# Performance work log

Measured on AMD Instinct MI355X. Metric: run time of the kernel, lower is better.

## Reference

```python
import jax, jax.numpy as jnp
import numpy as np

N_NODES = 50000
N_EDGES = 1600000
IN_DIM = 128
HIDDEN = 256
N_CLASSES = 2
N_GRAPHS = 512
BN_EPS = 1e-5


def setup_inputs() -> dict:
    key = jax.random.key(0)
    ks = jax.random.split(key, 12)
    x = jax.random.normal(ks[0], (N_NODES, IN_DIM), dtype=jnp.float32)
    edge_index = jax.random.randint(ks[1], (2, N_EDGES), 0, N_NODES, dtype=jnp.int64)
    batch = jnp.sort(jax.random.randint(ks[2], (N_NODES,), 0, N_GRAPHS, dtype=jnp.int64))
    s1 = 1.0 / np.sqrt(IN_DIM)
    s2 = 1.0 / np.sqrt(HIDDEN)
    return {
        "x": x,
        "edge_index": edge_index,
        "batch": batch,
        # GIN MLP: Linear(in,hidden) -> BN -> ReLU -> Linear(hidden,hidden)
        "W1": jax.random.uniform(ks[3], (IN_DIM, HIDDEN), jnp.float32, -s1, s1),
        "b1": jnp.zeros((HIDDEN,), jnp.float32),
        "g1": jnp.ones((HIDDEN,), jnp.float32),
        "be1": jnp.zeros((HIDDEN,), jnp.float32),
        "W2": jax.random.uniform(ks[4], (HIDDEN, HIDDEN), jnp.float32, -s2, s2),
        "b2": jnp.zeros((HIDDEN,), jnp.float32),
        # attention gate: Linear(hidden, 1)
        "Wg": jax.random.uniform(ks[5], (HIDDEN, 1), jnp.float32, -s2, s2),
        "bg": jnp.zeros((1,), jnp.float32),
        # head: BN(hidden) -> Dropout(eval: identity) -> Linear(hidden, n_classes)
        "g2": jnp.ones((HIDDEN,), jnp.float32),
        "be2": jnp.zeros((HIDDEN,), jnp.float32),
        "Wh": jax.random.uniform(ks[6], (HIDDEN, N_CLASSES), jnp.float32, -s2, s2),
        "bh": jnp.zeros((N_CLASSES,), jnp.float32),
    }


def _batchnorm(h, gamma, beta):
    # training-mode BN: batch statistics over axis 0 (biased variance, as torch)
    mu = jnp.mean(h, axis=0)
    var = jnp.mean(jnp.square(h - mu), axis=0)
    return gamma * (h - mu) * jax.lax.rsqrt(var + BN_EPS) + beta


def reference(x, edge_index, batch, W1, b1, g1, be1, W2, b2, Wg, bg, g2, be2, Wh, bh):
    src, dst = edge_index[0], edge_index[1]
    # GINConv (eps=0): agg_i = sum_{j->i} x_j ; h = MLP(x + agg)
    agg = jax.ops.segment_sum(x[src], dst, num_segments=N_NODES)  # [N, in_dim]
    h = x + agg
    h = h @ W1 + b1                      # [N, hidden]
    h = jax.nn.relu(_batchnorm(h, g1, be1))
    h = h @ W2 + b2                      # [N, hidden]
    h = jax.nn.relu(h)                   # outer F.relu in forward
    # AttentionalAggregation: segment softmax of gate, weighted sum per graph
    gate = h @ Wg + bg                   # [N, 1]
    m = jax.ops.segment_max(gate, batch, num_segments=N_GRAPHS)  # [G, 1]
    e = jnp.exp(gate - m[batch])
    s = jax.ops.segment_sum(e, batch, num_segments=N_GRAPHS)     # [G, 1]
    alpha = e / s[batch]                 # [N, 1]
    pooled = jax.ops.segment_sum(alpha * h, batch, num_segments=N_GRAPHS)  # [G, hidden]
    # head: BN -> (Dropout eval = identity) -> Linear -> log_softmax
    z = _batchnorm(pooled, g2, be2) @ Wh + bh  # [G, n_classes]
    return jax.nn.log_softmax(z, axis=-1)
```

## Files before the change

kernel.cpp:

```cpp
#include <hip/hip_runtime.h>

typedef unsigned int u32;
typedef unsigned short ushort_t;
typedef __attribute__((ext_vector_type(8))) short bf16x8;
typedef __attribute__((ext_vector_type(4))) float f32x4;

__device__ __forceinline__ float bf2f_lo(u32 u){
  union{u32 i; float f;} v; v.i = u<<16; return v.f;
}
__device__ __forceinline__ float bf2f_hi(u32 u){
  union{u32 i; float f;} v; v.i = u & 0xFFFF0000u; return v.f;
}
__device__ __forceinline__ float bf2f_s(ushort_t u){
  union{u32 i; float f;} v; v.i = ((u32)u)<<16; return v.f;
}
__device__ __forceinline__ u32 pack2bf(float a, float b){
  union{float f; u32 i;} va, vb; va.f=a; vb.f=b;
  u32 ra = (va.i + 0x7FFF + ((va.i>>16)&1)) >> 16;
  u32 rb = (vb.i + 0x7FFF + ((vb.i>>16)&1)) & 0xFFFF0000u;
  return ra | rb;
}
__device__ __forceinline__ ushort_t f2bf1(float f){
  union{float f; u32 i;} v; v.f=f;
  u32 r = v.i + 0x7FFF + ((v.i>>16)&1);
  return (ushort_t)(r>>16);
}

__global__ __launch_bounds__(256) void to_bf16(const float* __restrict__ x, u32* __restrict__ xb, long n4){
  long i = (long)blockIdx.x*256 + threadIdx.x;
  if(i*4 >= n4*4) return;
  float4 v = ((const float4*)x)[i];
  uint2 o; o.x = pack2bf(v.x, v.y); o.y = pack2bf(v.z, v.w);
  ((uint2*)xb)[i] = o;
}

__global__ __launch_bounds__(256) void transpose_w(const float* __restrict__ W, ushort_t* __restrict__ Wt, int K){
  int n = blockIdx.x;
  for(int k = threadIdx.x; k < K; k += 256){
    Wt[(size_t)n*K + k] = f2bf1(W[(size_t)k*256 + n]);
  }
}

__global__ __launch_bounds__(256) void hist_k(const int* __restrict__ dst, int* __restrict__ bcount,
                                              int E, int N, int NB){
  __shared__ int h[1024];
  for(int i=threadIdx.x; i<1024; i+=256) h[i]=0;
  __syncthreads();
  int e0 = blockIdx.x*8192;
  int e1 = min(e0+8192, E);
  for(int i=e0+threadIdx.x; i<e1; i+=256){
    int d = dst[i];
    if((u32)d >= (u32)N) d = 0;
    atomicAdd(&h[d>>6], 1);
  }
  __syncthreads();
  for(int i=threadIdx.x; i<NB; i+=256){
    int v = h[i];
    if(v) atomicAdd(&bcount[i], v);
  }
}

__global__ __launch_bounds__(256) void bucket_scan(const int* __restrict__ bcount, int* __restrict__ bstart,
                                                   int* __restrict__ bcursor, int* __restrict__ offs,
                                                   int NB, int N, int E){
  __shared__ int tsum[256];
  int t = threadIdx.x;
  int base = t*4;
  int a0 = (base+0<NB)?bcount[base+0]:0;
  int a1 = (base+1<NB)?bcount[base+1]:0;
  int a2 = (base+2<NB)?bcount[base+2]:0;
  int a3 = (base+3<NB)?bcount[base+3]:0;
  int s0=a0, s1=s0+a1, s2=s1+a2, s3=s2+a3;
  tsum[t]=s3; __syncthreads();
  #pragma unroll
  for(int d=1; d<256; d<<=1){
    int v = (t>=d)?tsum[t-d]:0;
    __syncthreads();
    tsum[t]+=v;
    __syncthreads();
  }
  int prev = (t>0)?tsum[t-1]:0;
  if(base+0<NB){ bstart[base+0]=prev;    bcursor[(base+0)*16]=0; }
  if(base+1<NB){ bstart[base+1]=prev+s0; bcursor[(base+1)*16]=0; }
  if(base+2<NB){ bstart[base+2]=prev+s1; bcursor[(base+2)*16]=0; }
  if(base+3<NB){ bstart[base+3]=prev+s2; bcursor[(base+3)*16]=0; }
  if(t==255){ bstart[NB]=prev+s3; offs[N]=E; }
}

__global__ __launch_bounds__(256) void binscatter2(const int* __restrict__ src, const int* __restrict__ dst,
                                                   const int* __restrict__ bstart, int* __restrict__ bcursor,
                                                   u32* __restrict__ pairs, int E, int N, int NB){
  __shared__ int hist[1024];
  __shared__ int base[1024];
  int e0 = blockIdx.x*8192;
  int e1 = min(e0+8192, E);
  for(int i=threadIdx.x; i<NB; i+=256) hist[i]=0;
  __syncthreads();
  for(int i=e0+threadIdx.x; i<e1; i+=256){
    int d = dst[i];
    if((u32)d >= (u32)N) d = 0;
    atomicAdd(&hist[d>>6], 1);
  }
  __syncthreads();
  for(int i=threadIdx.x; i<NB; i+=256){
    int c = hist[i];
    base[i] = c ? (bstart[i] + atomicAdd(&bcursor[i*16], c)) : 0;
    hist[i] = 0;
  }
  __syncthreads();
  for(int i=e0+threadIdx.x; i<e1; i+=256){
    int d = dst[i]; if((u32)d >= (u32)N) d = 0;
    int s = src[i]; if((u32)s >= (u32)N) s = 0;
    int b = d>>6;
    int loc = atomicAdd(&hist[b], 1);
    pairs[base[b]+loc] = (u32)s | (((u32)(d & 63))<<17);
  }
}

__global__ __launch_bounds__(256) void bucket_csr(const u32* __restrict__ pairs, const int* __restrict__ bstart,
                                                  int* __restrict__ offs, int* __restrict__ elist, int N){
  __shared__ int dcnt[64];
  __shared__ int dcur[64];
  int b = blockIdx.x;
  int p0 = bstart[b], p1 = bstart[b+1];
  if(threadIdx.x < 64) dcnt[threadIdx.x] = 0;
  __syncthreads();
  for(int i=p0+threadIdx.x; i<p1; i+=256){
    u32 u = pairs[i];
    atomicAdd(&dcnt[u>>17], 1);
  }
  __syncthreads();
  if(threadIdx.x == 0){
    int running = p0;
    #pragma unroll
    for(int j=0;j<64;j++){
      dcur[j] = running;
      int node = b*64 + j;
      if(node < N) offs[node] = running;
      running += dcnt[j];
    }
  }
  __syncthreads();
  for(int i=p0+threadIdx.x; i<p1; i+=256){
    u32 u = pairs[i];
    int pos = atomicAdd(&dcur[u>>17], 1);
    elist[pos] = (int)(u & 0x1FFFFu);
  }
}

__global__ __launch_bounds__(256) void gather_sum_bf(const u32* __restrict__ xb, const int* __restrict__ offs,
                                                     const int* __restrict__ elist, u32* __restrict__ h0b,
                                                     int N, int E){
  int slot = threadIdx.x >> 4;
  int c = threadIdx.x & 15;
  int i = blockIdx.x*16 + slot;
  if(i >= N) return;
  const uint4* xr = (const uint4*)xb;
  uint4 xv = xr[(size_t)i*16 + c];
  float acc[8] = {
    bf2f_lo(xv.x), bf2f_hi(xv.x), bf2f_lo(xv.y), bf2f_hi(xv.y),
    bf2f_lo(xv.z), bf2f_hi(xv.z), bf2f_lo(xv.w), bf2f_hi(xv.w) };
  int e0 = offs[i], e1 = offs[i+1];
  e0 = max(0, min(e0, E));
  e1 = max(e0, min(e1, E));
  int j = e0;
  for(; j+4 <= e1; j += 4){
    int s0 = elist[j+0]; if((u32)s0 >= (u32)N) s0 = 0;
    int s1 = elist[j+1]; if((u32)s1 >= (u32)N) s1 = 0;
    int s2 = elist[j+2]; if((u32)s2 >= (u32)N) s2 = 0;
    int s3 = elist[j+3]; if((u32)s3 >= (u32)N) s3 = 0;
    uint4 v0 = xr[(size_t)s0*16 + c];
    uint4 v1 = xr[(size_t)s1*16 + c];
    uint4 v2 = xr[(size_t)s2*16 + c];
    uint4 v3 = xr[(size_t)s3*16 + c];
    acc[0]+=bf2f_lo(v0.x); acc[1]+=bf2f_hi(v0.x); acc[2]+=bf2f_lo(v0.y); acc[3]+=bf2f_hi(v0.y);
    acc[4]+=bf2f_lo(v0.z); acc[5]+=bf2f_hi(v0.z); acc[6]+=bf2f_lo(v0.w); acc[7]+=bf2f_hi(v0.w);
    acc[0]+=bf2f_lo(v1.x); acc[1]+=bf2f_hi(v1.x); acc[2]+=bf2f_lo(v1.y); acc[3]+=bf2f_hi(v1.y);
    acc[4]+=bf2f_lo(v1.z); acc[5]+=bf2f_hi(v1.z); acc[6]+=bf2f_lo(v1.w); acc[7]+=bf2f_hi(v1.w);
    acc[0]+=bf2f_lo(v2.x); acc[1]+=bf2f_hi(v2.x); acc[2]+=bf2f_lo(v2.y); acc[3]+=bf2f_hi(v2.y);
    acc[4]+=bf2f_lo(v2.z); acc[5]+=bf2f_hi(v2.z); acc[6]+=bf2f_lo(v2.w); acc[7]+=bf2f_hi(v2.w);
    acc[0]+=bf2f_lo(v3.x); acc[1]+=bf2f_hi(v3.x); acc[2]+=bf2f_lo(v3.y); acc[3]+=bf2f_hi(v3.y);
    acc[4]+=bf2f_lo(v3.z); acc[5]+=bf2f_hi(v3.z); acc[6]+=bf2f_lo(v3.w); acc[7]+=bf2f_hi(v3.w);
  }
  for(; j < e1; j++){
    int s = elist[j];
    if((u32)s >= (u32)N) s = 0;
    uint4 v = xr[(size_t)s*16 + c];
    acc[0]+=bf2f_lo(v.x); acc[1]+=bf2f_hi(v.x);
    acc[2]+=bf2f_lo(v.y); acc[3]+=bf2f_hi(v.y);
    acc[4]+=bf2f_lo(v.z); acc[5]+=bf2f_hi(v.z);
    acc[6]+=bf2f_lo(v.w); acc[7]+=bf2f_hi(v.w);
  }
  uint4 o;
  o.x = pack2bf(acc[0],acc[1]); o.y = pack2bf(acc[2],acc[3]);
  o.z = pack2bf(acc[4],acc[5]); o.w = pack2bf(acc[6],acc[7]);
  ((uint4*)h0b)[(size_t)i*16 + c] = o;
}

template<int K, bool BNA, bool RELUOUT, bool GATE, bool ABF16, bool OUTBF16>
__global__ __launch_bounds__(512) void gemm_mfma(const void* __restrict__ Ap, const ushort_t* __restrict__ Wt,
                                                 const float* __restrict__ bias,
                                                 const float* __restrict__ scale, const float* __restrict__ shift,
                                                 void* __restrict__ Cp, int M,
                                                 const float* __restrict__ Wg, const float* __restrict__ bg,
                                                 float* __restrict__ gate){
  __shared__ uint4 Al[8*129];
  __shared__ uint4 Bl[8*257];
  __shared__ float gacc[128];
  const int tid  = threadIdx.x;
  const int lane = tid & 63;
  const int wave = tid >> 6;
  const int lm   = lane & 15;
  const int q    = lane >> 4;
  const int mhalf= wave >> 2;
  const int nq   = wave & 3;
  const int m0   = blockIdx.x * 128;

  if(GATE && tid < 128) gacc[tid] = 0.f;

  f32x4 acc[4][4];
  #pragma unroll
  for(int i=0;i<4;i++)
    #pragma unroll
    for(int j=0;j<4;j++) acc[i][j] = (f32x4){0.f,0.f,0.f,0.f};

  for(int k0=0; k0<K; k0+=64){
    #pragma unroll
    for(int i=0;i<2;i++){
      int idx = tid*2 + i;
      int m = idx >> 3, c = idx & 7;
      int grow = m0 + m;
      int kk = k0 + c*8;
      uint4 v = make_uint4(0,0,0,0);
      if(ABF16){
        if(grow < M) v = *(const uint4*)((const ushort_t*)Ap + (size_t)grow*K + kk);
        if(BNA){
          float f0=bf2f_lo(v.x), f1=bf2f_hi(v.x), f2=bf2f_lo(v.y), f3=bf2f_hi(v.y);
          float f4=bf2f_lo(v.z), f5=bf2f_hi(v.z), f6=bf2f_lo(v.w), f7=bf2f_hi(v.w);
          float4 s0 = *(const float4*)(scale+kk),  s1 = *(const float4*)(scale+kk+4);
          float4 t0 = *(const float4*)(shift+kk),  t1 = *(const float4*)(shift+kk+4);
          f0=fmaxf(fmaf(s0.x,f0,t0.x),0.f); f1=fmaxf(fmaf(s0.y,f1,t0.y),0.f);
          f2=fmaxf(fmaf(s0.z,f2,t0.z),0.f); f3=fmaxf(fmaf(s0.w,f3,t0.w),0.f);
          f4=fmaxf(fmaf(s1.x,f4,t1.x),0.f); f5=fmaxf(fmaf(s1.y,f5,t1.y),0.f);
          f6=fmaxf(fmaf(s1.z,f6,t1.z),0.f); f7=fmaxf(fmaf(s1.w,f7,t1.w),0.f);
          v.x = pack2bf(f0,f1); v.y = pack2bf(f2,f3);
          v.z = pack2bf(f4,f5); v.w = pack2bf(f6,f7);
        }
      } else {
        float4 u0 = make_float4(0,0,0,0), u1 = make_float4(0,0,0,0);
        if(grow < M){
          u0 = *(const float4*)((const float*)Ap + (size_t)grow*K + kk);
          u1 = *(const float4*)((const float*)Ap + (size_t)grow*K + kk + 4);
        }
        if(BNA){
          float4 s0 = *(const float4*)(scale+kk),  s1 = *(const float4*)(scale+kk+4);
          float4 t0 = *(const float4*)(shift+kk),  t1 = *(const float4*)(shift+kk+4);
          u0.x=fmaxf(fmaf(s0.x,u0.x,t0.x),0.f); u0.y=fmaxf(fmaf(s0.y,u0.y,t0.y),0.f);
          u0.z=fmaxf(fmaf(s0.z,u0.z,t0.z),0.f); u0.w=fmaxf(fmaf(s0.w,u0.w,t0.w),0.f);
          u1.x=fmaxf(fmaf(s1.x,u1.x,t1.x),0.f); u1.y=fmaxf(fmaf(s1.y,u1.y,t1.y),0.f);
          u1.z=fmaxf(fmaf(s1.z,u1.z,t1.z),0.f); u1.w=fmaxf(fmaf(s1.w,u1.w,t1.w),0.f);
        }
        v.x = pack2bf(u0.x,u0.y); v.y = pack2bf(u0.z,u0.w);
        v.z = pack2bf(u1.x,u1.y); v.w = pack2bf(u1.z,u1.w);
      }
      Al[c*129 + m] = v;
    }
    #pragma unroll
    for(int i=0;i<4;i++){
      int idx = tid*4 + i;
      int n = idx >> 3, c = idx & 7;
      Bl[c*257 + n] = *(const uint4*)(Wt + (size_t)n*K + k0 + c*8);
    }
    __syncthreads();
    #pragma unroll
    for(int ks=0; ks<2; ks++){
      int cc = ks*4 + q;
      bf16x8 af[4], bfr[4];
      #pragma unroll
      for(int mi=0; mi<4; mi++)
        af[mi] = *((const bf16x8*)&Al[cc*129 + mhalf*64 + mi*16 + lm]);
      #pragma unroll
      for(int ni=0; ni<4; ni++)
        bfr[ni] = *((const bf16x8*)&Bl[cc*257 + nq*64 + ni*16 + lm]);
      #pragma unroll
      for(int mi=0; mi<4; mi++)
        #pragma unroll
        for(int ni=0; ni<4; ni++)
          acc[mi][ni] = __builtin_amdgcn_mfma_f32_16x16x32_bf16(af[mi], bfr[ni], acc[mi][ni], 0, 0, 0);
    }
    __syncthreads();
  }

  float bb[4], wgv[4];
  #pragma unroll
  for(int ni=0; ni<4; ni++){
    int col = nq*64 + ni*16 + lm;
    bb[ni] = bias[col];
    if(GATE) wgv[ni] = Wg[col];
  }
  #pragma unroll
  for(int mi=0; mi<4; mi++){
    int rowloc0 = mhalf*64 + mi*16 + q*4;
    float gp[4] = {0.f,0.f,0.f,0.f};
    #pragma unroll
    for(int ni=0; ni<4; ni++){
      int col = nq*64 + ni*16 + lm;
      f32x4 o = acc[mi][ni];
      #pragma unroll
      for(int r=0; r<4; r++){
        float v = o[r] + bb[ni];
        if(RELUOUT) v = fmaxf(v, 0.f);
        int row = m0 + rowloc0 + r;
        if(row < M){
          if(OUTBF16) ((ushort_t*)Cp)[(size_t)row*256 + col] = f2bf1(v);
          else        ((float*)Cp)[(size_t)row*256 + col] = v;
        }
        if(GATE) gp[r] = fmaf(v, wgv[ni], gp[r]);
      }
    }
    if(GATE){
      #pragma unroll
      for(int r=0; r<4; r++){
        if(m0 + rowloc0 + r < M) atomicAdd(&gacc[rowloc0 + r], gp[r]);
      }
    }
  }
  if(GATE){
    __syncthreads();
    if(tid < 128){
      int row = m0 + tid;
      if(row < M) gate[row] = gacc[tid] + bg[0];
    }
  }
}

__global__ __launch_bounds__(256) void col_stats_bf(const u32* __restrict__ h, float* __restrict__ psum,
                                                    float* __restrict__ pq, int M, int rpb, int nblk){
  int b = blockIdx.x;
  int g = threadIdx.x >> 6;
  int lane = threadIdx.x & 63;
  int c0 = lane*4;
  int r0 = b*rpb;
  int r1 = min(r0+rpb, M);
  float4 s4 = make_float4(0.f,0.f,0.f,0.f);
  float4 q4 = make_float4(0.f,0.f,0.f,0.f);
  for(int r=r0+g; r<r1; r+=4){
    uint2 u = *(const uint2*)(h + (size_t)r*128 + lane*2);
    float v0=bf2f_lo(u.x), v1=bf2f_hi(u.x), v2=bf2f_lo(u.y), v3=bf2f_hi(u.y);
    s4.x+=v0; s4.y+=v1; s4.z+=v2; s4.w+=v3;
    q4.x=fmaf(v0,v0,q4.x); q4.y=fmaf(v1,v1,q4.y);
    q4.z=fmaf(v2,v2,q4.z); q4.w=fmaf(v3,v3,q4.w);
  }
  __shared__ float ls[1024];
  __shared__ float lq[1024];
  *(float4*)&ls[g*256+c0] = s4;
  *(float4*)&lq[g*256+c0] = q4;
  __syncthreads();
  if(threadIdx.x < 64){
    #pragma unroll
    for(int j=0;j<4;j++){
      int c = c0+j;
      float s = ls[c]+ls[256+c]+ls[512+c]+ls[768+c];
      float q = lq[c]+lq[256+c]+lq[512+c]+lq[768+c];
      psum[(size_t)c*nblk + b] = s;
      pq[(size_t)c*nblk + b]   = q;
    }
  }
}

__global__ __launch_bounds__(256) void col_stats2(const float* __restrict__ h, float* __restrict__ psum,
                                                  float* __restrict__ pq, int M, int rpb, int nblk){
  int b = blockIdx.x;
  int g = threadIdx.x >> 6;
  int lane = threadIdx.x & 63;
  int c0 = lane*4;
  int r0 = b*rpb;
  int r1 = min(r0+rpb, M);
  float4 s4 = make_float4(0.f,0.f,0.f,0.f);
  float4 q4 = make_float4(0.f,0.f,0.f,0.f);
  for(int r=r0+g; r<r1; r+=4){
    float4 v = *(const float4*)(h + (size_t)r*256 + c0);
    s4.x+=v.x; s4.y+=v.y; s4.z+=v.z; s4.w+=v.w;
    q4.x=fmaf(v.x,v.x,q4.x); q4.y=fmaf(v.y,v.y,q4.y);
    q4.z=fmaf(v.z,v.z,q4.z); q4.w=fmaf(v.w,v.w,q4.w);
  }
  __shared__ float ls[1024];
  __shared__ float lq[1024];
  *(float4*)&ls[g*256+c0] = s4;
  *(float4*)&lq[g*256+c0] = q4;
  __syncthreads();
  if(threadIdx.x < 64){
    #pragma unroll
    for(int j=0;j<4;j++){
      int c = c0+j;
      float s = ls[c]+ls[256+c]+ls[512+c]+ls[768+c];
      float q = lq[c]+lq[256+c]+lq[512+c]+lq[768+c];
      psum[(size_t)c*nblk + b] = s;
      pq[(size_t)c*nblk + b]   = q;
    }
  }
}

__global__ __launch_bounds__(512) void stats_fin(const float* __restrict__ psum, const float* __restrict__ pq,
                                                 const float* __restrict__ gamma, const float* __restrict__ beta,
                                                 float* __restrict__ scale, float* __restrict__ shift,
                                                 int nblk, float invM){
  __shared__ float red[512];
  int t = threadIdx.x;
  const float* src = (t<256) ? (psum + (size_t)t*nblk) : (pq + (size_t)(t-256)*nblk);
  float s = 0.f;
  for(int i=0;i<nblk;i+=4){
    float4 v = *(const float4*)(src+i);
    s += v.x+v.y+v.z+v.w;
  }
  red[t]=s; __syncthreads();
  if(t<256){
    float mu  = red[t]*invM;
    float var = fmaxf(red[256+t]*invM - mu*mu, 0.f);
    float sc  = gamma[t] * rsqrtf(var + 1e-5f);
    scale[t]=sc; shift[t]=fmaf(-mu, sc, beta[t]);
  }
}

__global__ __launch_bounds__(256) void pool_k(const ushort_t* __restrict__ h2b, const float* __restrict__ gate,
                                              const int* __restrict__ batch, float* __restrict__ pooled, int N){
  int g = blockIdx.x;
  __shared__ int sb[2];
  __shared__ float red[4];
  __shared__ float s_m, s_inv;
  if(threadIdx.x < 2){
    int target = g + threadIdx.x;
    int lo=0, hi=N;
    while(lo<hi){ int mid=(lo+hi)>>1; if(batch[mid] < target) lo=mid+1; else hi=mid; }
    sb[threadIdx.x] = lo;
  }
  __syncthreads();
  int beg = sb[0], end = sb[1];
  float mx = -1e30f;
  for(int i=beg+threadIdx.x; i<end; i+=256) mx = fmaxf(mx, gate[i]);
  #pragma unroll
  for(int d=32; d>0; d>>=1) mx = fmaxf(mx, __shfl_down(mx, d, 64));
  if((threadIdx.x&63)==0) red[threadIdx.x>>6] = mx;
  __syncthreads();
  if(threadIdx.x==0) s_m = fmaxf(fmaxf(red[0],red[1]), fmaxf(red[2],red[3]));
  __syncthreads();
  float m = s_m;
  float s = 0.f;
  for(int i=beg+threadIdx.x; i<end; i+=256) s += expf(gate[i]-m);
  #pragma unroll
  for(int d=32; d>0; d>>=1) s += __shfl_down(s, d, 64);
  if((threadIdx.x&63)==0) red[threadIdx.x>>6] = s;
  __syncthreads();
  if(threadIdx.x==0){
    float tot = red[0]+red[1]+red[2]+red[3];
    s_inv = (tot > 0.f) ? 1.f/tot : 0.f;
  }
  __syncthreads();
  float inv = s_inv;
  int t = threadIdx.x;
  float acc = 0.f;
  int i = beg;
  for(; i+2 <= end; i += 2){
    float a0 = expf(gate[i]-m) * inv;
    float a1 = expf(gate[i+1]-m) * inv;
    float h0 = bf2f_s(h2b[(size_t)i*256 + t]);
    float h1 = bf2f_s(h2b[(size_t)(i+1)*256 + t]);
    acc = fmaf(a0, h0, acc);
    acc = fmaf(a1, h1, acc);
  }
  for(; i < end; i++){
    float a = expf(gate[i]-m) * inv;
    acc = fmaf(a, bf2f_s(h2b[(size_t)i*256 + t]), acc);
  }
  pooled[g*256 + t] = acc;
}

__global__ __launch_bounds__(256) void head_k(const float* __restrict__ pooled,
                                              const float* __restrict__ sc2, const float* __restrict__ sh2,
                                              const float* __restrict__ Wh, const float* __restrict__ bh,
                                              float* __restrict__ out, int G){
  int w = (blockIdx.x*256 + threadIdx.x) >> 6;
  int l = threadIdx.x & 63;
  if(w >= G) return;
  float4 v  = *(const float4*)(pooled + (size_t)w*256 + l*4);
  float4 sc = *(const float4*)(sc2 + l*4);
  float4 sh = *(const float4*)(sh2 + l*4);
  float vv[4] = { fmaf(sc.x,v.x,sh.x), fmaf(sc.y,v.y,sh.y), fmaf(sc.z,v.z,sh.z), fmaf(sc.w,v.w,sh.w) };
  float4 w0 = *(const float4*)(Wh + (size_t)l*8);
  float4 w1 = *(const float4*)(Wh + (size_t)l*8 + 4);
  float a0 = vv[0]*w0.x + vv[1]*w0.z + vv[2]*w1.x + vv[3]*w1.z;
  float a1 = vv[0]*w0.y + vv[1]*w0.w + vv[2]*w1.y + vv[3]*w1.w;
  #pragma unroll
  for(int d=32; d>0; d>>=1){ a0 += __shfl_down(a0,d,64); a1 += __shfl_down(a1,d,64); }
  if(l==0){
    float z0 = a0 + bh[0];
    float z1 = a1 + bh[1];
    float mz = fmaxf(z0,z1);
    float lse = mz + logf(expf(z0-mz) + expf(z1-mz));
    out[w*2]   = z0 - lse;
    out[w*2+1] = z1 - lse;
  }
}

extern "C" void kernel_launch(void* const* d_in, const int* in_sizes, int n_in,
                              void* d_out, int out_size, void* d_ws, size_t ws_size,
                              hipStream_t stream){
  const float* x   = (const float*)d_in[0];
  const int*   ei  = (const int*)d_in[1];
  const int*   bat = (const int*)d_in[2];
  const float* W1  = (const float*)d_in[3];
  const float* b1  = (const float*)d_in[4];
  const float* g1  = (const float*)d_in[5];
  const float* be1 = (const float*)d_in[6];
  const float* W2  = (const float*)d_in[7];
  const float* b2  = (const float*)d_in[8];
  const float* Wg  = (const float*)d_in[9];
  const float* bg  = (const float*)d_in[10];
  const float* g2  = (const float*)d_in[11];
  const float* be2 = (const float*)d_in[12];
  const float* Wh  = (const float*)d_in[13];
  const float* bh  = (const float*)d_in[14];

  const int N = in_sizes[0] / 128;
  const int E = in_sizes[1] / 2;
  const int G = out_size / 2;
  const int NB = (N + 63) >> 6;
  const int NBLK1 = 512;
  const int NBLK2 = 64;

  char* ws = (char*)d_ws;
  u32*   h0b    = (u32*)ws;
  u32*   xb     = (u32*)(ws + 12800000);
  int*   elist  = (int*)(ws + 25600000);
  u32*   pairs  = (u32*)(ws + 32000000);
  int*   offs   = (int*)(ws + 38400000);
  int*   bcount = (int*)(ws + 38600192);
  int*   bstart = (int*)(ws + 38604288);
  int*   bcursor= (int*)(ws + 38608640);
  ushort_t* h2b = (ushort_t*)ws;
  u32*   h1b    = (u32*)(ws + 51200000);
  char*  p2 = ws + 102400000;
  float* psum1 = (float*)p2;          p2 += 256*NBLK1*4;
  float* pq1   = (float*)p2;          p2 += 256*NBLK1*4;
  float* psum2 = (float*)p2;          p2 += 256*NBLK2*4;
  float* pq2   = (float*)p2;          p2 += 256*NBLK2*4;
  float* sc1   = (float*)p2;          p2 += 1024;
  float* sh1   = (float*)p2;          p2 += 1024;
  float* gate  = (float*)p2;          p2 += (size_t)N*4 + 256;
  float* pooled= (float*)p2;          p2 += (size_t)G*256*4;
  float* sc2   = (float*)p2;          p2 += 1024;
  float* sh2   = (float*)p2;          p2 += 1024;
  ushort_t* W1t = (ushort_t*)p2;      p2 += 256*128*2;
  ushort_t* W2t = (ushort_t*)p2;      p2 += 256*256*2;

  const int* src = ei;
  const int* dst = ei + E;

  hipMemsetAsync(bcount, 0, (size_t)NB*4, stream);

  transpose_w<<<256, 256, 0, stream>>>(W1, W1t, 128);
  transpose_w<<<256, 256, 0, stream>>>(W2, W2t, 256);
  long n4 = (long)N*128/4;
  to_bf16    <<<(int)((n4+255)/256), 256, 0, stream>>>(x, xb, n4);

  int nchunk = (E + 8191)/8192;
  hist_k     <<<nchunk, 256, 0, stream>>>(dst, bcount, E, N, NB);
  bucket_scan<<<1, 256, 0, stream>>>(bcount, bstart, bcursor, offs, NB, N, E);
  binscatter2<<<nchunk, 256, 0, stream>>>(src, dst, bstart, bcursor, pairs, E, N, NB);
  bucket_csr <<<NB, 256, 0, stream>>>(pairs, bstart, offs, elist, N);
  gather_sum_bf<<<(N+15)/16, 256, 0, stream>>>(xb, offs, elist, h0b, N, E);

  int gblocks = (N + 127)/128;
  gemm_mfma<128,false,false,false,true,true><<<gblocks, 512, 0, stream>>>(
      h0b, W1t, b1, nullptr, nullptr, h1b, N, nullptr, nullptr, nullptr);
  int rpb1 = (N + NBLK1 - 1)/NBLK1;
  col_stats_bf <<<NBLK1, 256, 0, stream>>>(h1b, psum1, pq1, N, rpb1, NBLK1);
  stats_fin  <<<1, 512, 0, stream>>>(psum1, pq1, g1, be1, sc1, sh1, NBLK1, 1.0f/(float)N);
  gemm_mfma<256,true,true,true,true,true><<<gblocks, 512, 0, stream>>>(
      h1b, W2t, b2, sc1, sh1, h2b, N, Wg, bg, gate);

  pool_k <<<G, 256, 0, stream>>>(h2b, gate, bat, pooled, N);
  int rpb2 = (G + NBLK2 - 1)/NBLK2;
  col_stats2 <<<NBLK2, 256, 0, stream>>>(pooled, psum2, pq2, G, rpb2, NBLK2);
  stats_fin  <<<1, 512, 0, stream>>>(psum2, pq2, g2, be2, sc2, sh2, NBLK2, 1.0f/(float)G);
  head_k <<<(G+3)/4, 256, 0, stream>>>(pooled, sc2, sh2, Wh, bh, (float*)d_out, G);
}
```

Measured before the change: 362.9 us.

## Fuse bucket CSR build into gather and rework attention pooling

Merges the per-bucket CSR construction and the neighbor gather into one kernel. Each block sorts its bucket's edges into shared memory and then gathers the source rows directly, which removes the global elist/offs writes and reads and one kernel launch. The gather unrolls by 8 for more memory-level parallelism, and falls back to a slow linear scan when a bucket holds more than 4096 edges. Separately, pool_k moves to 512 threads, precomputes attention weights per chunk in shared memory and splits the rows across two halves, so the exp is computed once per node instead of once per thread.

```diff
diff --git a/kernel.cpp b/kernel.cpp
--- a/kernel.cpp
+++ b/kernel.cpp
@@ -61,8 +61,7 @@
 }
 
 __global__ __launch_bounds__(256) void bucket_scan(const int* __restrict__ bcount, int* __restrict__ bstart,
-                                                   int* __restrict__ bcursor, int* __restrict__ offs,
-                                                   int NB, int N, int E){
+                                                   int* __restrict__ bcursor, int NB){
   __shared__ int tsum[256];
   int t = threadIdx.x;
   int base = t*4;
@@ -84,7 +83,7 @@
   if(base+1<NB){ bstart[base+1]=prev+s0; bcursor[(base+1)*16]=0; }
   if(base+2<NB){ bstart[base+2]=prev+s1; bcursor[(base+2)*16]=0; }
   if(base+3<NB){ bstart[base+3]=prev+s2; bcursor[(base+3)*16]=0; }
-  if(t==255){ bstart[NB]=prev+s3; offs[N]=E; }
+  if(t==255){ bstart[NB]=prev+s3; }
 }
 
 __global__ __launch_bounds__(256) void binscatter2(const int* __restrict__ src, const int* __restrict__ dst,
@@ -117,84 +116,110 @@
   }
 }
 
-__global__ __launch_bounds__(256) void bucket_csr(const u32* __restrict__ pairs, const int* __restrict__ bstart,
-                                                  int* __restrict__ offs, int* __restrict__ elist, int N){
+#define BCAP 4096
+__global__ __launch_bounds__(256) void gather_bucket(const u32* __restrict__ xb,
+                                                     const u32* __restrict__ pairs,
+                                                     const int* __restrict__ bstart,
+                                                     u32* __restrict__ h0b, int N){
+  __shared__ int lsrc[BCAP];
   __shared__ int dcnt[64];
+  __shared__ int dstart[65];
   __shared__ int dcur[64];
   int b = blockIdx.x;
   int p0 = bstart[b], p1 = bstart[b+1];
-  if(threadIdx.x < 64) dcnt[threadIdx.x] = 0;
-  __syncthreads();
-  for(int i=p0+threadIdx.x; i<p1; i+=256){
-    u32 u = pairs[i];
-    atomicAdd(&dcnt[u>>17], 1);
-  }
-  __syncthreads();
-  if(threadIdx.x == 0){
-    int running = p0;
-    #pragma unroll
-    for(int j=0;j<64;j++){
-      dcur[j] = running;
-      int node = b*64 + j;
-      if(node < N) offs[node] = running;
-      running += dcnt[j];
-    }
-  }
-  __syncthreads();
-  for(int i=p0+threadIdx.x; i<p1; i+=256){
-    u32 u = pairs[i];
-    int pos = atomicAdd(&dcur[u>>17], 1);
-    elist[pos] = (int)(u & 0x1FFFFu);
-  }
-}
-
-__global__ __launch_bounds__(256) void gather_sum_bf(const u32* __restrict__ xb, const int* __restrict__ offs,
-                                                     const int* __restrict__ elist, u32* __restrict__ h0b,
-                                                     int N, int E){
-  int slot = threadIdx.x >> 4;
-  int c = threadIdx.x & 15;
-  int i = blockIdx.x*16 + slot;
-  if(i >= N) return;
+  int cnt = p1 - p0;
+  int tid = threadIdx.x;
+  if(tid < 64) dcnt[tid] = 0;
+  __syncthreads();
+  bool fits = (cnt <= BCAP) && (cnt >= 0);
+  if(fits){
+    for(int i=tid; i<cnt; i+=256){
+      u32 u = pairs[p0+i];
+      atomicAdd(&dcnt[(u>>17)&63], 1);
+    }
+    __syncthreads();
+    if(tid==0){
+      int run=0;
+      #pragma unroll
+      for(int j=0;j<64;j++){ dstart[j]=run; dcur[j]=run; run+=dcnt[j]; }
+      dstart[64]=run;
+    }
+    __syncthreads();
+    for(int i=tid; i<cnt; i+=256){
+      u32 u = pairs[p0+i];
+      int pos = atomicAdd(&dcur[(u>>17)&63], 1);
+      lsrc[pos] = (int)(u & 0x1FFFFu);
+    }
+    __syncthreads();
+  }
   const uint4* xr = (const uint4*)xb;
-  uint4 xv = xr[(size_t)i*16 + c];
-  float acc[8] = {
-    bf2f_lo(xv.x), bf2f_hi(xv.x), bf2f_lo(xv.y), bf2f_hi(xv.y),
-    bf2f_lo(xv.z), bf2f_hi(xv.z), bf2f_lo(xv.w), bf2f_hi(xv.w) };
-  int e0 = offs[i], e1 = offs[i+1];
-  e0 = max(0, min(e0, E));
-  e1 = max(e0, min(e1, E));
-  int j = e0;
-  for(; j+4 <= e1; j += 4){
-    int s0 = elist[j+0]; if((u32)s0 >= (u32)N) s0 = 0;
-    int s1 = elist[j+1]; if((u32)s1 >= (u32)N) s1 = 0;
-    int s2 = elist[j+2]; if((u32)s2 >= (u32)N) s2 = 0;
-    int s3 = elist[j+3]; if((u32)s3 >= (u32)N) s3 = 0;
-    uint4 v0 = xr[(size_t)s0*16 + c];
-    uint4 v1 = xr[(size_t)s1*16 + c];
-    uint4 v2 = xr[(size_t)s2*16 + c];
-    uint4 v3 = xr[(size_t)s3*16 + c];
-    acc[0]+=bf2f_lo(v0.x); acc[1]+=bf2f_hi(v0.x); acc[2]+=bf2f_lo(v0.y); acc[3]+=bf2f_hi(v0.y);
-    acc[4]+=bf2f_lo(v0.z); acc[5]+=bf2f_hi(v0.z); acc[6]+=bf2f_lo(v0.w); acc[7]+=bf2f_hi(v0.w);
-    acc[0]+=bf2f_lo(v1.x); acc[1]+=bf2f_hi(v1.x); acc[2]+=bf2f_lo(v1.y); acc[3]+=bf2f_hi(v1.y);
-    acc[4]+=bf2f_lo(v1.z); acc[5]+=bf2f_hi(v1.z); acc[6]+=bf2f_lo(v1.w); acc[7]+=bf2f_hi(v1.w);
-    acc[0]+=bf2f_lo(v2.x); acc[1]+=bf2f_hi(v2.x); acc[2]+=bf2f_lo(v2.y); acc[3]+=bf2f_hi(v2.y);
-    acc[4]+=bf2f_lo(v2.z); acc[5]+=bf2f_hi(v2.z); acc[6]+=bf2f_lo(v2.w); acc[7]+=bf2f_hi(v2.w);
-    acc[0]+=bf2f_lo(v3.x); acc[1]+=bf2f_hi(v3.x); acc[2]+=bf2f_lo(v3.y); acc[3]+=bf2f_hi(v3.y);
-    acc[4]+=bf2f_lo(v3.z); acc[5]+=bf2f_hi(v3.z); acc[6]+=bf2f_lo(v3.w); acc[7]+=bf2f_hi(v3.w);
-  }
-  for(; j < e1; j++){
-    int s = elist[j];
-    if((u32)s >= (u32)N) s = 0;
-    uint4 v = xr[(size_t)s*16 + c];
-    acc[0]+=bf2f_lo(v.x); acc[1]+=bf2f_hi(v.x);
-    acc[2]+=bf2f_lo(v.y); acc[3]+=bf2f_hi(v.y);
-    acc[4]+=bf2f_lo(v.z); acc[5]+=bf2f_hi(v.z);
-    acc[6]+=bf2f_lo(v.w); acc[7]+=bf2f_hi(v.w);
-  }
-  uint4 o;
-  o.x = pack2bf(acc[0],acc[1]); o.y = pack2bf(acc[2],acc[3]);
-  o.z = pack2bf(acc[4],acc[5]); o.w = pack2bf(acc[6],acc[7]);
-  ((uint4*)h0b)[(size_t)i*16 + c] = o;
+  int slot = tid >> 4;
+  int c = tid & 15;
+  for(int pass=0; pass<4; pass++){
+    int r = pass*16 + slot;
+    int node = b*64 + r;
+    if(node >= N) continue;
+    uint4 xv = xr[(size_t)node*16 + c];
+    float acc[8] = {
+      bf2f_lo(xv.x), bf2f_hi(xv.x), bf2f_lo(xv.y), bf2f_hi(xv.y),
+      bf2f_lo(xv.z), bf2f_hi(xv.z), bf2f_lo(xv.w), bf2f_hi(xv.w) };
+    if(fits){
+      int ds = dstart[r], de = dstart[r+1];
+      int j = ds;
+      for(; j+8 <= de; j += 8){
+        int s0=lsrc[j+0], s1=lsrc[j+1], s2=lsrc[j+2], s3=lsrc[j+3];
+        int s4=lsrc[j+4], s5=lsrc[j+5], s6=lsrc[j+6], s7=lsrc[j+7];
+        uint4 v0 = xr[(size_t)s0*16 + c];
+        uint4 v1 = xr[(size_t)s1*16 + c];
+        uint4 v2 = xr[(size_t)s2*16 + c];
+        uint4 v3 = xr[(size_t)s3*16 + c];
+        uint4 v4 = xr[(size_t)s4*16 + c];
+        uint4 v5 = xr[(size_t)s5*16 + c];
+        uint4 v6 = xr[(size_t)s6*16 + c];
+        uint4 v7 = xr[(size_t)s7*16 + c];
+        acc[0]+=bf2f_lo(v0.x)+bf2f_lo(v1.x)+bf2f_lo(v2.x)+bf2f_lo(v3.x)
+               +bf2f_lo(v4.x)+bf2f_lo(v5.x)+bf2f_lo(v6.x)+bf2f_lo(v7.x);
+        acc[1]+=bf2f_hi(v0.x)+bf2f_hi(v1.x)+bf2f_hi(v2.x)+bf2f_hi(v3.x)
+               +bf2f_hi(v4.x)+bf2f_hi(v5.x)+bf2f_hi(v6.x)+bf2f_hi(v7.x);
+        acc[2]+=bf2f_lo(v0.y)+bf2f_lo(v1.y)+bf2f_lo(v2.y)+bf2f_lo(v3.y)
+               +bf2f_lo(v4.y)+bf2f_lo(v5.y)+bf2f_lo(v6.y)+bf2f_lo(v7.y);
+        acc[3]+=bf2f_hi(v0.y)+bf2f_hi(v1.y)+bf2f_hi(v2.y)+bf2f_hi(v3.y)
+               +bf2f_hi(v4.y)+bf2f_hi(v5.y)+bf2f_hi(v6.y)+bf2f_hi(v7.y);
+        acc[4]+=bf2f_lo(v0.z)+bf2f_lo(v1.z)+bf2f_lo(v2.z)+bf2f_lo(v3.z)
+               +bf2f_lo(v4.z)+bf2f_lo(v5.z)+bf2f_lo(v6.z)+bf2f_lo(v7.z);
+        acc[5]+=bf2f_hi(v0.z)+bf2f_hi(v1.z)+bf2f_hi(v2.z)+bf2f_hi(v3.z)
+               +bf2f_hi(v4.z)+bf2f_hi(v5.z)+bf2f_hi(v6.z)+bf2f_hi(v7.z);
+        acc[6]+=bf2f_lo(v0.w)+bf2f_lo(v1.w)+bf2f_lo(v2.w)+bf2f_lo(v3.w)
+               +bf2f_lo(v4.w)+bf2f_lo(v5.w)+bf2f_lo(v6.w)+bf2f_lo(v7.w);
+        acc[7]+=bf2f_hi(v0.w)+bf2f_hi(v1.w)+bf2f_hi(v2.w)+bf2f_hi(v3.w)
+               +bf2f_hi(v4.w)+bf2f_hi(v5.w)+bf2f_hi(v6.w)+bf2f_hi(v7.w);
+      }
+      for(; j < de; j++){
+        int s = lsrc[j];
+        uint4 v = xr[(size_t)s*16 + c];
+        acc[0]+=bf2f_lo(v.x); acc[1]+=bf2f_hi(v.x);
+        acc[2]+=bf2f_lo(v.y); acc[3]+=bf2f_hi(v.y);
+        acc[4]+=bf2f_lo(v.z); acc[5]+=bf2f_hi(v.z);
+        acc[6]+=bf2f_lo(v.w); acc[7]+=bf2f_hi(v.w);
+      }
+    } else {
+      for(int i=0;i<cnt;i++){
+        u32 u = pairs[p0+i];
+        if((int)((u>>17)&63) == r){
+          int s = (int)(u & 0x1FFFFu);
+          uint4 v = xr[(size_t)s*16 + c];
+          acc[0]+=bf2f_lo(v.x); acc[1]+=bf2f_hi(v.x);
+          acc[2]+=bf2f_lo(v.y); acc[3]+=bf2f_hi(v.y);
+          acc[4]+=bf2f_lo(v.z); acc[5]+=bf2f_hi(v.z);
+          acc[6]+=bf2f_lo(v.w); acc[7]+=bf2f_hi(v.w);
+        }
+      }
+    }
+    uint4 o;
+    o.x = pack2bf(acc[0],acc[1]); o.y = pack2bf(acc[2],acc[3]);
+    o.z = pack2bf(acc[4],acc[5]); o.w = pack2bf(acc[6],acc[7]);
+    ((uint4*)h0b)[(size_t)node*16 + c] = o;
+  }
 }
 
 template<int K, bool BNA, bool RELUOUT, bool GATE, bool ABF16, bool OUTBF16>
@@ -422,57 +447,66 @@
   }
 }
 
-__global__ __launch_bounds__(256) void pool_k(const ushort_t* __restrict__ h2b, const float* __restrict__ gate,
+__global__ __launch_bounds__(512) void pool_k(const ushort_t* __restrict__ h2b, const float* __restrict__ gate,
                                               const int* __restrict__ batch, float* __restrict__ pooled, int N){
   int g = blockIdx.x;
   __shared__ int sb[2];
-  __shared__ float red[4];
+  __shared__ float red[8];
   __shared__ float s_m, s_inv;
-  if(threadIdx.x < 2){
-    int target = g + threadIdx.x;
+  __shared__ float la[256];
+  __shared__ float facc[512];
+  int t = threadIdx.x;
+  if(t < 2){
+    int target = g + t;
     int lo=0, hi=N;
     while(lo<hi){ int mid=(lo+hi)>>1; if(batch[mid] < target) lo=mid+1; else hi=mid; }
-    sb[threadIdx.x] = lo;
+    sb[t] = lo;
   }
   __syncthreads();
   int beg = sb[0], end = sb[1];
   float mx = -1e30f;
-  for(int i=beg+threadIdx.x; i<end; i+=256) mx = fmaxf(mx, gate[i]);
+  for(int i=beg+t; i<end; i+=512) mx = fmaxf(mx, gate[i]);
   #pragma unroll
   for(int d=32; d>0; d>>=1) mx = fmaxf(mx, __shfl_down(mx, d, 64));
-  if((threadIdx.x&63)==0) red[threadIdx.x>>6] = mx;
-  __syncthreads();
-  if(threadIdx.x==0) s_m = fmaxf(fmaxf(red[0],red[1]), fmaxf(red[2],red[3]));
+  if((t&63)==0) red[t>>6] = mx;
+  __syncthreads();
+  if(t==0){
+    float m = red[0];
+    #pragma unroll
+    for(int w=1; w<8; w++) m = fmaxf(m, red[w]);
+    s_m = m;
+  }
   __syncthreads();
   float m = s_m;
   float s = 0.f;
-  for(int i=beg+threadIdx.x; i<end; i+=256) s += expf(gate[i]-m);
+  for(int i=beg+t; i<end; i+=512) s += expf(gate[i]-m);
   #pragma unroll
   for(int d=32; d>0; d>>=1) s += __shfl_down(s, d, 64);
-  if((threadIdx.x&63)==0) red[threadIdx.x>>6] = s;
-  __syncthreads();
-  if(threadIdx.x==0){
-    float tot = red[0]+red[1]+red[2]+red[3];
+  if((t&63)==0) red[t>>6] = s;
+  __syncthreads();
+  if(t==0){
+    float tot = 0.f;
+    #pragma unroll
+    for(int w=0; w<8; w++) tot += red[w];
     s_inv = (tot > 0.f) ? 1.f/tot : 0.f;
   }
   __syncthreads();
   float inv = s_inv;
-  int t = threadIdx.x;
+  int col = t & 255;
+  int half = t >> 8;
   float acc = 0.f;
-  int i = beg;
-  for(; i+2 <= end; i += 2){
-    float a0 = expf(gate[i]-m) * inv;
-    float a1 = expf(gate[i+1]-m) * inv;
-    float h0 = bf2f_s(h2b[(size_t)i*256 + t]);
-    float h1 = bf2f_s(h2b[(size_t)(i+1)*256 + t]);
-    acc = fmaf(a0, h0, acc);
-    acc = fmaf(a1, h1, acc);
-  }
-  for(; i < end; i++){
-    float a = expf(gate[i]-m) * inv;
-    acc = fmaf(a, bf2f_s(h2b[(size_t)i*256 + t]), acc);
-  }
-  pooled[g*256 + t] = acc;
+  for(int ci=beg; ci<end; ci+=256){
+    int chunk = min(256, end-ci);
+    if(t < 256) la[t] = (t < chunk) ? expf(gate[ci+t]-m)*inv : 0.f;
+    __syncthreads();
+    for(int j=half; j<chunk; j+=2){
+      acc = fmaf(la[j], bf2f_s(h2b[(size_t)(ci+j)*256 + col]), acc);
+    }
+    __syncthreads();
+  }
+  facc[t] = acc;
+  __syncthreads();
+  if(t < 256) pooled[g*256 + t] = facc[t] + facc[t+256];
 }
 
 __global__ __launch_bounds__(256) void head_k(const float* __restrict__ pooled,
@@ -531,12 +565,10 @@
   char* ws = (char*)d_ws;
   u32*   h0b    = (u32*)ws;
   u32*   xb     = (u32*)(ws + 12800000);
-  int*   elist  = (int*)(ws + 25600000);
-  u32*   pairs  = (u32*)(ws + 32000000);
-  int*   offs   = (int*)(ws + 38400000);
-  int*   bcount = (int*)(ws + 38600192);
-  int*   bstart = (int*)(ws + 38604288);
-  int*   bcursor= (int*)(ws + 38608640);
+  u32*   pairs  = (u32*)(ws + 25600000);
+  int*   bcount = (int*)(ws + 32000000);
+  int*   bstart = (int*)(ws + 32004352);
+  int*   bcursor= (int*)(ws + 32008704);
   ushort_t* h2b = (ushort_t*)ws;
   u32*   h1b    = (u32*)(ws + 51200000);
   char*  p2 = ws + 102400000;
@@ -546,7 +578,7 @@
   float* pq2   = (float*)p2;          p2 += 256*NBLK2*4;
   float* sc1   = (float*)p2;          p2 += 1024;
   float* sh1   = (float*)p2;          p2 += 1024;
-  float* gate  = (float*)p2;          p2 += (size_t)N*4 + 256;
+  float* gate  = (float*)p2;          p2 += (size_t)N*4 + 4096;
   float* pooled= (float*)p2;          p2 += (size_t)G*256*4;
   float* sc2   = (float*)p2;          p2 += 1024;
   float* sh2   = (float*)p2;          p2 += 1024;
@@ -565,10 +597,9 @@
 
   int nchunk = (E + 8191)/8192;
   hist_k     <<<nchunk, 256, 0, stream>>>(dst, bcount, E, N, NB);
-  bucket_scan<<<1, 256, 0, stream>>>(bcount, bstart, bcursor, offs, NB, N, E);
+  bucket_scan<<<1, 256, 0, stream>>>(bcount, bstart, bcursor, NB);
   binscatter2<<<nchunk, 256, 0, stream>>>(src, dst, bstart, bcursor, pairs, E, N, NB);
-  bucket_csr <<<NB, 256, 0, stream>>>(pairs, bstart, offs, elist, N);
-  gather_sum_bf<<<(N+15)/16, 256, 0, stream>>>(xb, offs, elist, h0b, N, E);
+  gather_bucket<<<NB, 256, 0, stream>>>(xb, pairs, bstart, h0b, N);
 
   int gblocks = (N + 127)/128;
   gemm_mfma<128,false,false,false,true,true><<<gblocks, 512, 0, stream>>>(
@@ -579,7 +610,7 @@
   gemm_mfma<256,true,true,true,true,true><<<gblocks, 512, 0, stream>>>(
       h1b, W2t, b2, sc1, sh1, h2b, N, Wg, bg, gate);
 
-  pool_k <<<G, 256, 0, stream>>>(h2b, gate, bat, pooled, N);
+  pool_k <<<G, 512, 0, stream>>>(h2b, gate, bat, pooled, N);
   int rpb2 = (G + NBLK2 - 1)/NBLK2;
   col_stats2 <<<NBLK2, 256, 0, stream>>>(pooled, psum2, pq2, G, rpb2, NBLK2);
   stats_fin  <<<1, 512, 0, stream>>>(psum2, pq2, g2, be2, sc2, sh2, NBLK2, 1.0f/(float)G);
```

Measured after the change: 355.6 us. 2.0% less time.
